# Kernel optimization log

Measured on AMD Instinct MI355X. Metric: run time of the kernel, lower is better.

## Reference

```python
import jax, jax.numpy as jnp
import numpy as np

B, F, E, T = 4, 128, 3000, 6000  # batch, features, input edges, unroll_target


def setup_inputs() -> dict:
    key = jax.random.key(0)
    k1, k2 = jax.random.split(key)
    features = jax.random.normal(k1, (B, F, E), dtype=jnp.float32)
    # Sparse one-hot-like group matrix: each padded group matrix is binary with
    # a few nonzeros per target column (as produced by mesh.get_groups + pad_groups).
    unroll_mat = (jax.random.uniform(k2, (B, E, T)) < (2.0 / E)).astype(jnp.float32)
    # occurrences[b, t] = number of times target edge t occurs across groups;
    # pad_occurrences pads with 1, so clamp to a minimum of 1.
    occurrences = jnp.maximum(unroll_mat.sum(axis=1), 1.0)  # (B, T)
    return {"features": features, "unroll_mat": unroll_mat, "occurrences": occurrences}


def reference(features, unroll_mat, occurrences):
    # unroll_mat: (B, E, T) padded group matrix; occurrences: (B, T)
    # normalized mapping, then dense bmm: (B,F,E) @ (B,E,T) -> (B,F,T)
    norm_mat = unroll_mat / occurrences[:, None, :]
    return jnp.einsum('bfe,bet->bft', features, norm_mat)
```

## Files before the change

kernel.cpp:

```cpp
#include <hip/hip_runtime.h>

#define B 4
#define F 128
#define E 3000
#define T 6000
#define K 16
#define ECHUNK 40
#define CAP 1024

typedef unsigned int u32x4 __attribute__((ext_vector_type(4)));

__global__ __launch_bounds__(256) void feat_transpose_kernel(
        const float* __restrict__ features, float* __restrict__ ft) {
    __shared__ float tile[32][33];
    const int b  = blockIdx.z;
    const int e0 = blockIdx.x * 32;
    const int f0 = blockIdx.y * 32;
    const int tx = threadIdx.x;
    const int ty = threadIdx.y;
    const float* fb = features + (size_t)b * F * E;
    float* ob = ft + (size_t)b * E * F;
#pragma unroll
    for (int j = 0; j < 4; ++j) {
        const int f = f0 + ty + 8 * j;
        const int e = e0 + tx;
        tile[ty + 8 * j][tx] = (e < E) ? fb[(size_t)f * E + e] : 0.0f;
    }
    __syncthreads();
#pragma unroll
    for (int j = 0; j < 4; ++j) {
        const int e = e0 + ty + 8 * j;
        const int f = f0 + tx;
        if (e < E) ob[(size_t)e * F + f] = tile[tx][ty + 8 * j];
    }
}

__global__ __launch_bounds__(256, 8) void unpool_scan_kernel(
        const float* __restrict__ unroll,
        int* __restrict__ counts,
        int* __restrict__ idx) {
    __shared__ int ls_cnt;
    __shared__ int2 ls_buf[CAP];

    const int b  = blockIdx.z;
    const int e0 = blockIdx.y * ECHUNK;
    const int t4 = (blockIdx.x * blockDim.x + threadIdx.x) * 4;
    const bool active = (t4 + 3) < T;

    if (threadIdx.x == 0) ls_cnt = 0;
    __syncthreads();

    const float* base = unroll + (size_t)b * E * T + t4;
    int* cbase = counts + b * T;
    int* ibase = idx + (size_t)b * T * K;

    if (active) {
#define LROW(e) __builtin_nontemporal_load(reinterpret_cast<const u32x4*>(base + (size_t)(e) * T))
#define PROC(v, ee)                                                                  \
    do {                                                                             \
        const unsigned nz = (v[0] | v[1] | v[2] | v[3]);                             \
        if (__ballot(nz != 0u)) {                                                    \
            if (v[0]) { int s = atomicAdd(&ls_cnt, 1); if (s < CAP) ls_buf[s] = make_int2(t4 + 0, (ee)); } \
            if (v[1]) { int s = atomicAdd(&ls_cnt, 1); if (s < CAP) ls_buf[s] = make_int2(t4 + 1, (ee)); } \
            if (v[2]) { int s = atomicAdd(&ls_cnt, 1); if (s < CAP) ls_buf[s] = make_int2(t4 + 2, (ee)); } \
            if (v[3]) { int s = atomicAdd(&ls_cnt, 1); if (s < CAP) ls_buf[s] = make_int2(t4 + 3, (ee)); } \
        }                                                                            \
    } while (0)

        u32x4 c0 = LROW(e0 + 0), c1 = LROW(e0 + 1), c2 = LROW(e0 + 2), c3 = LROW(e0 + 3);
#pragma unroll 1
        for (int eg = 0; eg < ECHUNK - 4; eg += 4) {
            const int e = e0 + eg;
            u32x4 n0 = LROW(e + 4), n1 = LROW(e + 5), n2 = LROW(e + 6), n3 = LROW(e + 7);
            PROC(c0, e + 0);
            PROC(c1, e + 1);
            PROC(c2, e + 2);
            PROC(c3, e + 3);
            c0 = n0; c1 = n1; c2 = n2; c3 = n3;
        }
        const int el = e0 + ECHUNK - 4;
        PROC(c0, el + 0);
        PROC(c1, el + 1);
        PROC(c2, el + 2);
        PROC(c3, el + 3);
#undef PROC
#undef LROW
    }

    __syncthreads();
    const int n = ls_cnt;
    if (n <= CAP) {
        for (int i = threadIdx.x; i < n; i += 256) {
            const int2 p = ls_buf[i];
            const int c = atomicAdd(&cbase[p.x], 1);
            if (c < K) ibase[(size_t)p.x * K + c] = p.y;
        }
    } else if (active) {
        for (int e = e0; e < e0 + ECHUNK; ++e) {
            const float4 v = *reinterpret_cast<const float4*>(base + (size_t)e * T);
            if (v.x != 0.0f) { int c = atomicAdd(&cbase[t4 + 0], 1); if (c < K) ibase[(size_t)(t4 + 0) * K + c] = e; }
            if (v.y != 0.0f) { int c = atomicAdd(&cbase[t4 + 1], 1); if (c < K) ibase[(size_t)(t4 + 1) * K + c] = e; }
            if (v.z != 0.0f) { int c = atomicAdd(&cbase[t4 + 2], 1); if (c < K) ibase[(size_t)(t4 + 2) * K + c] = e; }
            if (v.w != 0.0f) { int c = atomicAdd(&cbase[t4 + 3], 1); if (c < K) ibase[(size_t)(t4 + 3) * K + c] = e; }
        }
    }
}

__global__ __launch_bounds__(256) void unpool_gather_kernel(
        const float* __restrict__ ft,
        const float* __restrict__ occ,
        const float* __restrict__ unroll,
        const int* __restrict__ counts,
        const int* __restrict__ idx,
        float* __restrict__ out) {
    const int b  = blockIdx.z;
    const int t  = blockIdx.x * 256 + threadIdx.x;
    const int f0 = blockIdx.y * 32;
    if (t >= T) return;

    const int c = counts[b * T + t];
    const float inv = 1.0f / occ[b * T + t];
    const float* fb = ft + (size_t)b * E * F;
    float* ob = out + (size_t)b * F * T + t;

    if (c <= K) {
        int es[K];
        const int4* ip4 = reinterpret_cast<const int4*>(idx + ((size_t)b * T + t) * K);
#pragma unroll
        for (int q = 0; q < 4; ++q) {
            const int4 v = ip4[q];
            es[4 * q + 0] = v.x; es[4 * q + 1] = v.y;
            es[4 * q + 2] = v.z; es[4 * q + 3] = v.w;
        }
#pragma unroll
        for (int j = 0; j < 8; ++j) {
            const int f = f0 + 4 * j;
            float4 a = make_float4(0.f, 0.f, 0.f, 0.f);
#pragma unroll
            for (int k = 0; k < K; ++k) {
                if (k < c) {
                    const float4 v = *reinterpret_cast<const float4*>(fb + (size_t)es[k] * F + f);
                    a.x += v.x; a.y += v.y; a.z += v.z; a.w += v.w;
                }
            }
            ob[(size_t)(f + 0) * T] = a.x * inv;
            ob[(size_t)(f + 1) * T] = a.y * inv;
            ob[(size_t)(f + 2) * T] = a.z * inv;
            ob[(size_t)(f + 3) * T] = a.w * inv;
        }
    } else {
        for (int j = 0; j < 8; ++j) {
            const int f = f0 + 4 * j;
            float4 a = make_float4(0.f, 0.f, 0.f, 0.f);
            for (int e = 0; e < E; ++e) {
                if (unroll[((size_t)b * E + e) * T + t] != 0.0f) {
                    const float4 v = *reinterpret_cast<const float4*>(fb + (size_t)e * F + f);
                    a.x += v.x; a.y += v.y; a.z += v.z; a.w += v.w;
                }
            }
            ob[(size_t)(f + 0) * T] = a.x * inv;
            ob[(size_t)(f + 1) * T] = a.y * inv;
            ob[(size_t)(f + 2) * T] = a.z * inv;
            ob[(size_t)(f + 3) * T] = a.w * inv;
        }
    }
}

__global__ void unpool_dense_fallback(const float* __restrict__ features,
                                      const float* __restrict__ unroll,
                                      const float* __restrict__ occ,
                                      float* __restrict__ out) {
    const int b = blockIdx.z;
    const int f = blockIdx.y;
    const int t = blockIdx.x * 64 + threadIdx.x;
    if (t >= T) return;
    const float* frow = features + ((size_t)b * F + f) * E;
    const float* ub = unroll + (size_t)b * E * T;
    float acc = 0.0f;
    for (int e = 0; e < E; ++e) acc += frow[e] * ub[(size_t)e * T + t];
    out[((size_t)b * F + f) * T + t] = acc / occ[b * T + t];
}

extern "C" void kernel_launch(void* const* d_in, const int* in_sizes, int n_in,
                              void* d_out, int out_size, void* d_ws, size_t ws_size,
                              hipStream_t stream) {
    const float* features = (const float*)d_in[0];
    const float* unroll   = (const float*)d_in[1];
    const float* occ      = (const float*)d_in[2];
    float* out = (float*)d_out;

    const size_t counts_bytes = (size_t)B * T * sizeof(int);
    const size_t idx_bytes    = (size_t)B * T * K * sizeof(int);
    const size_t ft_bytes     = (size_t)B * E * F * sizeof(float);

    if (ws_size < counts_bytes + idx_bytes + ft_bytes) {
        dim3 g((T + 63) / 64, F, B);
        unpool_dense_fallback<<<g, 64, 0, stream>>>(features, unroll, occ, out);
        return;
    }

    int*   counts = (int*)d_ws;
    int*   idx    = counts + (size_t)B * T;
    float* ft     = (float*)(idx + (size_t)B * T * K);

    hipMemsetAsync(counts, 0, counts_bytes, stream);

    dim3 gt((E + 31) / 32, F / 32, B);
    feat_transpose_kernel<<<gt, dim3(32, 8), 0, stream>>>(features, ft);

    dim3 g1((T / 4 + 255) / 256, E / ECHUNK, B);
    unpool_scan_kernel<<<g1, 256, 0, stream>>>(unroll, counts, idx);

    dim3 g2((T + 255) / 256, F / 32, B);
    unpool_gather_kernel<<<g2, 256, 0, stream>>>(ft, occ, unroll, counts, idx, out);
}
```

Baseline: 84.89 us.

## Fold counts zeroing into transpose, use plain loads in scan, halve gather feature tile

The separate memset of the counts buffer is removed, and the transpose kernel now zeroes counts using its global thread index. The grid has 94*4*4*256 threads, more than B*T entries, so every entry is covered. The scan kernel switches from nontemporal vector loads to plain float4 loads and drops its occupancy hint from launch bounds. The gather kernel now covers 16 features per block instead of 32, doubling the number of blocks, and writes its output with nontemporal stores. Together these aim to cut a launch and improve occupancy, at the cost of gathering each index list twice as often.

Result: faster. 71.36 us (-15.9%).

```diff
diff --git a/kernel.cpp b/kernel.cpp
--- a/kernel.cpp
+++ b/kernel.cpp
@@ -8,16 +8,22 @@
 #define ECHUNK 40
 #define CAP 1024
 
-typedef unsigned int u32x4 __attribute__((ext_vector_type(4)));
-
 __global__ __launch_bounds__(256) void feat_transpose_kernel(
-        const float* __restrict__ features, float* __restrict__ ft) {
+        const float* __restrict__ features, float* __restrict__ ft,
+        int* __restrict__ counts) {
     __shared__ float tile[32][33];
     const int b  = blockIdx.z;
     const int e0 = blockIdx.x * 32;
     const int f0 = blockIdx.y * 32;
     const int tx = threadIdx.x;
     const int ty = threadIdx.y;
+
+    {
+        const int blk = (blockIdx.z * gridDim.y + blockIdx.y) * gridDim.x + blockIdx.x;
+        const int gtid = blk * 256 + ty * 32 + tx;
+        if (gtid < B * T) counts[gtid] = 0;
+    }
+
     const float* fb = features + (size_t)b * F * E;
     float* ob = ft + (size_t)b * E * F;
 #pragma unroll
@@ -35,7 +41,7 @@
     }
 }
 
-__global__ __launch_bounds__(256, 8) void unpool_scan_kernel(
+__global__ __launch_bounds__(256) void unpool_scan_kernel(
         const float* __restrict__ unroll,
         int* __restrict__ counts,
         int* __restrict__ idx) {
@@ -55,23 +61,24 @@
     int* ibase = idx + (size_t)b * T * K;
 
     if (active) {
-#define LROW(e) __builtin_nontemporal_load(reinterpret_cast<const u32x4*>(base + (size_t)(e) * T))
+#define LROW(e) (*reinterpret_cast<const float4*>(base + (size_t)(e) * T))
+#define ANY_NZ(v) ((__float_as_uint(v.x) | __float_as_uint(v.y) | \
+                    __float_as_uint(v.z) | __float_as_uint(v.w)) != 0u)
 #define PROC(v, ee)                                                                  \
     do {                                                                             \
-        const unsigned nz = (v[0] | v[1] | v[2] | v[3]);                             \
-        if (__ballot(nz != 0u)) {                                                    \
-            if (v[0]) { int s = atomicAdd(&ls_cnt, 1); if (s < CAP) ls_buf[s] = make_int2(t4 + 0, (ee)); } \
-            if (v[1]) { int s = atomicAdd(&ls_cnt, 1); if (s < CAP) ls_buf[s] = make_int2(t4 + 1, (ee)); } \
-            if (v[2]) { int s = atomicAdd(&ls_cnt, 1); if (s < CAP) ls_buf[s] = make_int2(t4 + 2, (ee)); } \
-            if (v[3]) { int s = atomicAdd(&ls_cnt, 1); if (s < CAP) ls_buf[s] = make_int2(t4 + 3, (ee)); } \
+        if (__ballot(ANY_NZ(v))) {                                                   \
+            if (v.x != 0.0f) { int s = atomicAdd(&ls_cnt, 1); if (s < CAP) ls_buf[s] = make_int2(t4 + 0, (ee)); } \
+            if (v.y != 0.0f) { int s = atomicAdd(&ls_cnt, 1); if (s < CAP) ls_buf[s] = make_int2(t4 + 1, (ee)); } \
+            if (v.z != 0.0f) { int s = atomicAdd(&ls_cnt, 1); if (s < CAP) ls_buf[s] = make_int2(t4 + 2, (ee)); } \
+            if (v.w != 0.0f) { int s = atomicAdd(&ls_cnt, 1); if (s < CAP) ls_buf[s] = make_int2(t4 + 3, (ee)); } \
         }                                                                            \
     } while (0)
 
-        u32x4 c0 = LROW(e0 + 0), c1 = LROW(e0 + 1), c2 = LROW(e0 + 2), c3 = LROW(e0 + 3);
+        float4 c0 = LROW(e0 + 0), c1 = LROW(e0 + 1), c2 = LROW(e0 + 2), c3 = LROW(e0 + 3);
 #pragma unroll 1
         for (int eg = 0; eg < ECHUNK - 4; eg += 4) {
             const int e = e0 + eg;
-            u32x4 n0 = LROW(e + 4), n1 = LROW(e + 5), n2 = LROW(e + 6), n3 = LROW(e + 7);
+            float4 n0 = LROW(e + 4), n1 = LROW(e + 5), n2 = LROW(e + 6), n3 = LROW(e + 7);
             PROC(c0, e + 0);
             PROC(c1, e + 1);
             PROC(c2, e + 2);
@@ -84,6 +91,7 @@
         PROC(c2, el + 2);
         PROC(c3, el + 3);
 #undef PROC
+#undef ANY_NZ
 #undef LROW
     }
 
@@ -115,7 +123,7 @@
         float* __restrict__ out) {
     const int b  = blockIdx.z;
     const int t  = blockIdx.x * 256 + threadIdx.x;
-    const int f0 = blockIdx.y * 32;
+    const int f0 = blockIdx.y * 16;
     if (t >= T) return;
 
     const int c = counts[b * T + t];
@@ -133,7 +141,7 @@
             es[4 * q + 2] = v.z; es[4 * q + 3] = v.w;
         }
 #pragma unroll
-        for (int j = 0; j < 8; ++j) {
+        for (int j = 0; j < 4; ++j) {
             const int f = f0 + 4 * j;
             float4 a = make_float4(0.f, 0.f, 0.f, 0.f);
 #pragma unroll
@@ -143,13 +151,13 @@
                     a.x += v.x; a.y += v.y; a.z += v.z; a.w += v.w;
                 }
             }
-            ob[(size_t)(f + 0) * T] = a.x * inv;
-            ob[(size_t)(f + 1) * T] = a.y * inv;
-            ob[(size_t)(f + 2) * T] = a.z * inv;
-            ob[(size_t)(f + 3) * T] = a.w * inv;
+            __builtin_nontemporal_store(a.x * inv, ob + (size_t)(f + 0) * T);
+            __builtin_nontemporal_store(a.y * inv, ob + (size_t)(f + 1) * T);
+            __builtin_nontemporal_store(a.z * inv, ob + (size_t)(f + 2) * T);
+            __builtin_nontemporal_store(a.w * inv, ob + (size_t)(f + 3) * T);
         }
     } else {
-        for (int j = 0; j < 8; ++j) {
+        for (int j = 0; j < 4; ++j) {
             const int f = f0 + 4 * j;
             float4 a = make_float4(0.f, 0.f, 0.f, 0.f);
             for (int e = 0; e < E; ++e) {
@@ -203,14 +211,12 @@
     int*   idx    = counts + (size_t)B * T;
     float* ft     = (float*)(idx + (size_t)B * T * K);
 
-    hipMemsetAsync(counts, 0, counts_bytes, stream);
-
     dim3 gt((E + 31) / 32, F / 32, B);
-    feat_transpose_kernel<<<gt, dim3(32, 8), 0, stream>>>(features, ft);
+    feat_transpose_kernel<<<gt, dim3(32, 8), 0, stream>>>(features, ft, counts);
 
     dim3 g1((T / 4 + 255) / 256, E / ECHUNK, B);
     unpool_scan_kernel<<<g1, 256, 0, stream>>>(unroll, counts, idx);
 
-    dim3 g2((T + 255) / 256, F / 32, B);
+    dim3 g2((T + 255) / 256, F / 16, B);
     unpool_gather_kernel<<<g2, 256, 0, stream>>>(ft, occ, unroll, counts, idx, out);
 }
```
